# Kernel optimization log

Measured on AMD Instinct MI355X. Metric: run time of the kernel, lower is better.

## Reference

```python
import jax, jax.numpy as jnp
import numpy as np

EPISODES = 1_000_000


def setup_inputs() -> dict:
    key = jax.random.key(0)
    x = jax.random.normal(key, (1, EPISODES, 2), dtype=jnp.float32)
    return {"x": x}


def _rx_2x2(t):
    # expm(-i * t * X) = cos(t) I - i sin(t) X  (closed form for Pauli-X rotation)
    c = jnp.cos(t).astype(jnp.complex64)
    s = (-1j * jnp.sin(t).astype(jnp.complex64))
    row0 = jnp.stack([c, s], axis=-1)
    row1 = jnp.stack([s, c], axis=-1)
    return jnp.stack([row0, row1], axis=-2)  # (..., 2, 2)


def reference(x):
    # x: (1, E, 2) float32 -> angles a (qubit 1, X(x)I) and b (qubit 2, I(x)X)
    cnot = jnp.array([[1, 0, 0, 0],
                      [0, 1, 0, 0],
                      [0, 0, 0, 1],
                      [0, 0, 1, 0]], dtype=jnp.complex64)
    a = x[..., 0]  # (1, E)
    b = x[..., 1]  # (1, E)
    # sx1 = X(x)I and sx2 = I(x)X commute, so
    # expm(-i (a*sx1 + b*sx2)) = Rx(a) (x) Rx(b)  -- exact, replaces generic expm.
    Ra = _rx_2x2(a)  # (1, E, 2, 2)
    Rb = _rx_2x2(b)  # (1, E, 2, 2)
    # Kronecker product -> (1, E, 4, 4) complex64
    Rx = (Ra[..., :, None, :, None] * Rb[..., None, :, None, :]).reshape(
        a.shape[0], a.shape[1], 4, 4)
    propagator = jnp.einsum('iq,beqp->beip', cnot, Rx)  # (1, E, 4, 4)
    state_out = propagator[..., 0]                      # column 0 -> (1, E, 4)
    probabilities = jnp.square(jnp.abs(state_out)).astype(jnp.float32)
    logits = jnp.log(probabilities)                     # tf.log(prob) for multinomial
    # Vectorized categorical sampling over all episodes (replaces per-episode loop)
    skey = jax.random.key(42)
    choice = jax.random.categorical(skey, logits, axis=-1)  # (1, E) int
    # original: one_hot((1,1)) stacked on axis=1 -> (1, E, 1, 4)
    measurement = jax.nn.one_hot(choice, 4, dtype=jnp.float32)[:, :, None, :]
    return measurement
```

## Files before the change

### kernel.cpp

```cpp
#include <hip/hip_runtime.h>
#include <stdint.h>
#include <math.h>


#define N_EP 1000000

typedef float v2f __attribute__((ext_vector_type(2)));
#define V2(c) ((v2f){(c), (c)})

__device__ __forceinline__ uint32_t rotl32(uint32_t x, int d) {
  return (x << d) | (x >> (32 - d));
}

__device__ __forceinline__ void threefry(uint32_t x0, uint32_t x1,
                                         uint32_t& o0, uint32_t& o1) {
  const uint32_t k0 = 0u;
  const uint32_t k1 = 42u;
  const uint32_t k2 = (0u ^ 42u ^ 0x1BD11BDAu);
  x0 += k0; x1 += k1;
#define R4A { x0 += x1; x1 = rotl32(x1,13); x1 ^= x0; \
              x0 += x1; x1 = rotl32(x1,15); x1 ^= x0; \
              x0 += x1; x1 = rotl32(x1,26); x1 ^= x0; \
              x0 += x1; x1 = rotl32(x1, 6); x1 ^= x0; }
#define R4B { x0 += x1; x1 = rotl32(x1,17); x1 ^= x0; \
              x0 += x1; x1 = rotl32(x1,29); x1 ^= x0; \
              x0 += x1; x1 = rotl32(x1,16); x1 ^= x0; \
              x0 += x1; x1 = rotl32(x1,24); x1 ^= x0; }
  R4A; x0 += k1; x1 += k2 + 1u;
  R4B; x0 += k2; x1 += k0 + 2u;
  R4A; x0 += k0; x1 += k1 + 3u;
  R4B; x0 += k1; x1 += k2 + 4u;
  R4A; x0 += k2; x1 += k0 + 5u;
#undef R4A
#undef R4B
  o0 = x0; o1 = x1;
}


__device__ __forceinline__ v2f logf_xla2(v2f input) {
#pragma clang fp contract(off)
  const float kMinNorm = __uint_as_float(0x00800000u);
  uint32_t ubx = __float_as_uint(fmaxf(input.x, kMinNorm));
  uint32_t uby = __float_as_uint(fmaxf(input.y, kMinNorm));
  v2f e;
  e.x = (float)((int)(ubx >> 23) - 126);
  e.y = (float)((int)(uby >> 23) - 126);
  v2f x;
  x.x = __uint_as_float((ubx & 0x807fffffu) | 0x3f000000u);
  x.y = __uint_as_float((uby & 0x807fffffu) | 0x3f000000u);
  const float kSqrtHf = 0.707106781186547524f;
  bool mx = x.x < kSqrtHf;
  bool my = x.y < kSqrtHf;
  v2f tmp;
  tmp.x = mx ? x.x : 0.0f;
  tmp.y = my ? x.y : 0.0f;
  e.x = e.x - (mx ? 1.0f : 0.0f);
  e.y = e.y - (my ? 1.0f : 0.0f);
  x = x - V2(1.0f);
  x = x + tmp;
  v2f z = x * x;
  v2f y = V2(7.0376836292E-2f);
  y = y * x + V2(-1.1514610310E-1f);
  y = y * x + V2( 1.1676998740E-1f);
  y = y * x + V2(-1.2420140846E-1f);
  y = y * x + V2( 1.4249322787E-1f);
  y = y * x + V2(-1.6668057665E-1f);
  y = y * x + V2( 2.0000714765E-1f);
  y = y * x + V2(-2.4999993993E-1f);
  y = y * x + V2( 3.3333331174E-1f);
  y = y * x;
  y = y * z;
  y = e * V2(-2.12194440e-4f) + y;
  y = z * V2(-0.5f) + y;
  x = x + y;
  x = e * V2(0.693359375f) + x;
  if (input.x == 0.0f) x.x = -__builtin_inff();
  if (input.y == 0.0f) x.y = -__builtin_inff();
  return x;
}

__device__ __forceinline__ void sincosf_cr(float xf, float* sp, float* cp) {
  double x = (double)xf;
  double dn = __builtin_rint(x * 6.36619772367581382433e-01);
  int q = (int)dn;
  const double pio2_1  = 1.57079632673412561417e+00;
  const double pio2_1t = 6.07710050650619224932e-11;
  double r = fma(-dn, pio2_1, x);
  r = fma(-dn, pio2_1t, r);
  double z = r * r;
  double w = z * z;
  const double S1 = -1.66666666666666324348e-01;
  const double S2 =  8.33333333332248946124e-03;
  const double S3 = -1.98412698298579493134e-04;
  const double S4 =  2.75573137070700676789e-06;
  const double S5 = -2.50507602534068634195e-08;
  const double S6 =  1.58969099521155010221e-10;
  double rs = S2 + z * (S3 + z * S4) + z * w * (S5 + z * S6);
  double sinr = r + r * (z * (S1 + z * rs));
  const double C1 =  4.16666666666666019037e-02;
  const double C2 = -1.38888888888741095749e-03;
  const double C3 =  2.48015872894767294178e-05;
  const double C4 = -2.75573143513906633035e-07;
  const double C5 =  2.08757232129817482790e-09;
  const double C6 = -1.13596475577881948265e-11;
  double rc = z * (C1 + z * (C2 + z * C3)) + w * w * (C4 + z * (C5 + z * C6));
  double hz = 0.5 * z;
  double ww = 1.0 - hz;
  double cosr = ww + (((1.0 - ww) - hz) + z * rc);
  bool swap = q & 1;
  double s0 = swap ? cosr : sinr;
  double c0 = swap ? sinr : cosr;
  if (q & 2) s0 = -s0;
  if ((q + 1) & 2) c0 = -c0;
  *sp = (float)s0;
  *cp = (float)c0;
}

__device__ __forceinline__ float u_from_bits(uint32_t b) {
#pragma clang fp contract(off)
  const float tiny = 1.17549435e-38f;
  float f = __uint_as_float((b >> 9) | 0x3F800000u) - 1.0f;
  return fmaxf(tiny, f + tiny);
}

__device__ __forceinline__ v2f u2_from_bits(uint32_t b0, uint32_t b1) {
#pragma clang fp contract(off)
  const float tiny = 1.17549435e-38f;
  v2f f;
  f.x = __uint_as_float((b0 >> 9) | 0x3F800000u);
  f.y = __uint_as_float((b1 >> 9) | 0x3F800000u);
  f = f - V2(1.0f);
  f = f + V2(tiny);
  v2f u;
  u.x = fmaxf(tiny, f.x);
  u.y = fmaxf(tiny, f.y);
  return u;
}

__device__ __forceinline__ v2f gumbel2(uint32_t b0, uint32_t b1) {
  v2f u = u2_from_bits(b0, b1);
  v2f inner = logf_xla2(u);
  v2f outer = logf_xla2(-inner);
  return -outer;
}


__device__ __forceinline__ void fast_gumbel(uint32_t b, float* g, float* rtg) {
  const float LN2 = 0.6931471805599453f;
  float u = u_from_bits(b);
  float tg = -(LN2 * __builtin_amdgcn_logf(u));
  *g = -(LN2 * __builtin_amdgcn_logf(tg));
  *rtg = __builtin_amdgcn_rcpf(tg);
}

__global__ __launch_bounds__(256) void qcat_kernel(const float* __restrict__ x,
                                                   float* __restrict__ out) {
  int t = blockIdx.x * blockDim.x + threadIdx.x;
  if (t >= N_EP) return;

  uint32_t bits[4];
  uint32_t base = 4u * (uint32_t)t;
#pragma unroll
  for (int c = 0; c < 4; ++c) {
    uint32_t o0, o1;
    threefry(0u, base + (uint32_t)c, o0, o1);
    bits[c] = o0 ^ o1;
  }

  float2 ab = ((const float2*)x)[t];

  const float INV2PI = 0.15915494309189535f;
  const float LN2 = 0.6931471805599453f;
  float fra = __builtin_amdgcn_fractf(ab.x * INV2PI);
  float frb = __builtin_amdgcn_fractf(ab.y * INV2PI);
  float saf = __builtin_amdgcn_sinf(fra);
  float caf = __builtin_amdgcn_cosf(fra);
  float sbf = __builtin_amdgcn_sinf(frb);
  float cbf = __builtin_amdgcn_cosf(frb);
  float a0 = caf * cbf, a1 = caf * sbf, a2 = saf * sbf, a3 = saf * cbf;
  float p0 = a0 * a0, p1 = a1 * a1, p2 = a2 * a2, p3 = a3 * a3;
  float lp0 = LN2 * __builtin_amdgcn_logf(p0);
  float lp1 = LN2 * __builtin_amdgcn_logf(p1);
  float lp2 = LN2 * __builtin_amdgcn_logf(p2);
  float lp3 = LN2 * __builtin_amdgcn_logf(p3);
  float g0, g1, g2, g3, rtg0, rtg1, rtg2, rtg3;
  fast_gumbel(bits[0], &g0, &rtg0);
  fast_gumbel(bits[1], &g1, &rtg1);
  fast_gumbel(bits[2], &g2, &rtg2);
  fast_gumbel(bits[3], &g3, &rtg3);
  float y0 = lp0 + g0, y1 = lp1 + g1, y2 = lp2 + g2, y3 = lp3 + g3;

  const float K = 1.52587890625e-5f;
  float rta0 = __builtin_amdgcn_rcpf(fabsf(a0));
  float rta1 = __builtin_amdgcn_rcpf(fabsf(a1));
  float rta2 = __builtin_amdgcn_rcpf(fabsf(a2));
  float rta3 = __builtin_amdgcn_rcpf(fabsf(a3));
  float E0 = K * (fabsf(lp0) + fabsf(g0) + rtg0 + rta0 + 4.0f);
  float E1 = K * (fabsf(lp1) + fabsf(g1) + rtg1 + rta1 + 4.0f);
  float E2 = K * (fabsf(lp2) + fabsf(g2) + rtg2 + rta2 + 4.0f);
  float E3 = K * (fabsf(lp3) + fabsf(g3) + rtg3 + rta3 + 4.0f);
  float Emax = fmaxf(fmaxf(E0, E1), fmaxf(E2, E3));

  int   i01 = (y1 > y0) ? 1 : 0;
  float m01 = i01 ? y1 : y0;
  float s01 = i01 ? y0 : y1;
  int   i23 = (y3 > y2) ? 3 : 2;
  float m23 = i23 == 3 ? y3 : y2;
  float s23 = i23 == 3 ? y2 : y3;
  bool  sw  = m23 > m01;
  int   top = sw ? i23 : i01;
  float tv  = sw ? m23 : m01;
  float sv  = fmaxf(sw ? m01 : m23, sw ? s23 : s01);
  float margin = tv - sv;

  float pmin = fminf(fminf(p0, p1), fminf(p2, p3));
  bool safe = (margin > 2.0f * Emax) && (pmin >= 1.17549435e-38f);

  int best = top;
  if (!safe) {
#pragma clang fp contract(off)
    float ca, sa, cb, sb;
    sincosf_cr(ab.x, &sa, &ca);
    sincosf_cr(ab.y, &sb, &cb);
    v2f m0 = {ca, ca}, n0 = {cb, sb};
    v2f m1 = {sa, sa}, n1 = {sb, cb};
    v2f t01 = m0 * n0;
    v2f t23 = m1 * n1;
    v2f q01 = t01 * t01;
    v2f q23 = t23 * t23;
    v2f y01 = logf_xla2(q01) + gumbel2(bits[0], bits[1]);
    v2f y23 = logf_xla2(q23) + gumbel2(bits[2], bits[3]);
    int be = 0; float bv = y01.x;
    if (y01.y > bv) { bv = y01.y; be = 1; }
    if (y23.x > bv) { bv = y23.x; be = 2; }
    if (y23.y > bv) { bv = y23.y; be = 3; }
    best = be;
  }

  float4 o;
  o.x = (best == 0) ? 1.0f : 0.0f;
  o.y = (best == 1) ? 1.0f : 0.0f;
  o.z = (best == 2) ? 1.0f : 0.0f;
  o.w = (best == 3) ? 1.0f : 0.0f;
  ((float4*)out)[t] = o;
}

extern "C" void kernel_launch(void* const* d_in, const int* in_sizes, int n_in,
                              void* d_out, int out_size, void* d_ws, size_t ws_size,
                              hipStream_t stream) {
  const float* x = (const float*)d_in[0];
  float* out = (float*)d_out;
  dim3 block(256);
  dim3 grid((N_EP + 255) / 256);
  hipLaunchKernelGGL(qcat_kernel, grid, block, 0, stream, x, out);
}
```

Baseline: 73.28 us.

## Split unsafe episodes into atomic worklist and separate exact fixup kernel

The fast kernel no longer runs the exact double-precision sincos/log fallback inline. Instead it appends the indices of uncertain episodes to a workspace list through an atomic counter, and a separate fixup kernel recomputes only those episodes. The safety test also changes from a single global margin to per-pair error bounds, which should let more episodes count as safe. The aim is to remove divergent slow-path code and its register pressure from the main kernel. In exchange it adds two extra kernel launches and atomic contention, and the fixup grid of 64 blocks is fixed in size.

```diff
diff --git a/kernel.cpp b/kernel.cpp
--- a/kernel.cpp
+++ b/kernel.cpp
@@ -34,6 +34,13 @@
 #undef R4A
 #undef R4B
   o0 = x0; o1 = x1;
+}
+
+__device__ __forceinline__ float u_from_bits(uint32_t b) {
+#pragma clang fp contract(off)
+  const float tiny = 1.17549435e-38f;
+  float f = __uint_as_float((b >> 9) | 0x3F800000u) - 1.0f;
+  return fmaxf(tiny, f + tiny);
 }
 
 
@@ -116,13 +123,6 @@
   *cp = (float)c0;
 }
 
-__device__ __forceinline__ float u_from_bits(uint32_t b) {
-#pragma clang fp contract(off)
-  const float tiny = 1.17549435e-38f;
-  float f = __uint_as_float((b >> 9) | 0x3F800000u) - 1.0f;
-  return fmaxf(tiny, f + tiny);
-}
-
 __device__ __forceinline__ v2f u2_from_bits(uint32_t b0, uint32_t b1) {
 #pragma clang fp contract(off)
   const float tiny = 1.17549435e-38f;
@@ -145,16 +145,13 @@
 }
 
 
-__device__ __forceinline__ void fast_gumbel(uint32_t b, float* g, float* rtg) {
-  const float LN2 = 0.6931471805599453f;
-  float u = u_from_bits(b);
-  float tg = -(LN2 * __builtin_amdgcn_logf(u));
-  *g = -(LN2 * __builtin_amdgcn_logf(tg));
-  *rtg = __builtin_amdgcn_rcpf(tg);
-}
-
-__global__ __launch_bounds__(256) void qcat_kernel(const float* __restrict__ x,
-                                                   float* __restrict__ out) {
+__global__ void zero_ws(uint32_t* ws) {
+  if (blockIdx.x == 0 && threadIdx.x == 0) ws[0] = 0u;
+}
+
+__global__ __launch_bounds__(256) void fast_kernel(const float* __restrict__ x,
+                                                   float* __restrict__ out,
+                                                   uint32_t* __restrict__ ws) {
   int t = blockIdx.x * blockDim.x + threadIdx.x;
   if (t >= N_EP) return;
 
@@ -183,66 +180,99 @@
   float lp1 = LN2 * __builtin_amdgcn_logf(p1);
   float lp2 = LN2 * __builtin_amdgcn_logf(p2);
   float lp3 = LN2 * __builtin_amdgcn_logf(p3);
-  float g0, g1, g2, g3, rtg0, rtg1, rtg2, rtg3;
-  fast_gumbel(bits[0], &g0, &rtg0);
-  fast_gumbel(bits[1], &g1, &rtg1);
-  fast_gumbel(bits[2], &g2, &rtg2);
-  fast_gumbel(bits[3], &g3, &rtg3);
+
+  float u0 = u_from_bits(bits[0]);
+  float u1 = u_from_bits(bits[1]);
+  float u2 = u_from_bits(bits[2]);
+  float u3 = u_from_bits(bits[3]);
+  float tg0 = -(LN2 * __builtin_amdgcn_logf(u0));
+  float tg1 = -(LN2 * __builtin_amdgcn_logf(u1));
+  float tg2 = -(LN2 * __builtin_amdgcn_logf(u2));
+  float tg3 = -(LN2 * __builtin_amdgcn_logf(u3));
+  float g0 = -(LN2 * __builtin_amdgcn_logf(tg0));
+  float g1 = -(LN2 * __builtin_amdgcn_logf(tg1));
+  float g2 = -(LN2 * __builtin_amdgcn_logf(tg2));
+  float g3 = -(LN2 * __builtin_amdgcn_logf(tg3));
   float y0 = lp0 + g0, y1 = lp1 + g1, y2 = lp2 + g2, y3 = lp3 + g3;
 
   const float K = 1.52587890625e-5f;
-  float rta0 = __builtin_amdgcn_rcpf(fabsf(a0));
-  float rta1 = __builtin_amdgcn_rcpf(fabsf(a1));
-  float rta2 = __builtin_amdgcn_rcpf(fabsf(a2));
-  float rta3 = __builtin_amdgcn_rcpf(fabsf(a3));
-  float E0 = K * (fabsf(lp0) + fabsf(g0) + rtg0 + rta0 + 4.0f);
-  float E1 = K * (fabsf(lp1) + fabsf(g1) + rtg1 + rta1 + 4.0f);
-  float E2 = K * (fabsf(lp2) + fabsf(g2) + rtg2 + rta2 + 4.0f);
-  float E3 = K * (fabsf(lp3) + fabsf(g3) + rtg3 + rta3 + 4.0f);
-  float Emax = fmaxf(fmaxf(E0, E1), fmaxf(E2, E3));
-
-  int   i01 = (y1 > y0) ? 1 : 0;
-  float m01 = i01 ? y1 : y0;
-  float s01 = i01 ? y0 : y1;
-  int   i23 = (y3 > y2) ? 3 : 2;
-  float m23 = i23 == 3 ? y3 : y2;
-  float s23 = i23 == 3 ? y2 : y3;
-  bool  sw  = m23 > m01;
-  int   top = sw ? i23 : i01;
-  float tv  = sw ? m23 : m01;
-  float sv  = fmaxf(sw ? m01 : m23, sw ? s23 : s01);
-  float margin = tv - sv;
-
+  float E0 = K * (fabsf(lp0) + fabsf(g0) + __builtin_amdgcn_rcpf(tg0) +
+                  __builtin_amdgcn_rcpf(fabsf(a0)) + 4.0f);
+  float E1 = K * (fabsf(lp1) + fabsf(g1) + __builtin_amdgcn_rcpf(tg1) +
+                  __builtin_amdgcn_rcpf(fabsf(a1)) + 4.0f);
+  float E2 = K * (fabsf(lp2) + fabsf(g2) + __builtin_amdgcn_rcpf(tg2) +
+                  __builtin_amdgcn_rcpf(fabsf(a2)) + 4.0f);
+  float E3 = K * (fabsf(lp3) + fabsf(g3) + __builtin_amdgcn_rcpf(tg3) +
+                  __builtin_amdgcn_rcpf(fabsf(a3)) + 4.0f);
+
+  int best = 0; float bv = y0;
+  if (y1 > bv) { bv = y1; best = 1; }
+  if (y2 > bv) { bv = y2; best = 2; }
+  if (y3 > bv) { bv = y3; best = 3; }
+  float Eb = (best == 0) ? E0 : (best == 1) ? E1 : (best == 2) ? E2 : E3;
+
+  bool safe = true;
+  if (best != 0) safe = safe && (bv - y0 > Eb + E0);
+  if (best != 1) safe = safe && (bv - y1 > Eb + E1);
+  if (best != 2) safe = safe && (bv - y2 > Eb + E2);
+  if (best != 3) safe = safe && (bv - y3 > Eb + E3);
   float pmin = fminf(fminf(p0, p1), fminf(p2, p3));
-  bool safe = (margin > 2.0f * Emax) && (pmin >= 1.17549435e-38f);
-
-  int best = top;
-  if (!safe) {
-#pragma clang fp contract(off)
-    float ca, sa, cb, sb;
-    sincosf_cr(ab.x, &sa, &ca);
-    sincosf_cr(ab.y, &sb, &cb);
-    v2f m0 = {ca, ca}, n0 = {cb, sb};
-    v2f m1 = {sa, sa}, n1 = {sb, cb};
-    v2f t01 = m0 * n0;
-    v2f t23 = m1 * n1;
-    v2f q01 = t01 * t01;
-    v2f q23 = t23 * t23;
-    v2f y01 = logf_xla2(q01) + gumbel2(bits[0], bits[1]);
-    v2f y23 = logf_xla2(q23) + gumbel2(bits[2], bits[3]);
-    int be = 0; float bv = y01.x;
-    if (y01.y > bv) { bv = y01.y; be = 1; }
-    if (y23.x > bv) { bv = y23.x; be = 2; }
-    if (y23.y > bv) { bv = y23.y; be = 3; }
-    best = be;
+  safe = safe && (pmin >= 1.17549435e-38f);
+
+  if (safe) {
+    float4 o;
+    o.x = (best == 0) ? 1.0f : 0.0f;
+    o.y = (best == 1) ? 1.0f : 0.0f;
+    o.z = (best == 2) ? 1.0f : 0.0f;
+    o.w = (best == 3) ? 1.0f : 0.0f;
+    ((float4*)out)[t] = o;
+  } else {
+    uint32_t idx = atomicAdd(ws, 1u);
+    ws[4 + idx] = (uint32_t)t;
   }
-
-  float4 o;
-  o.x = (best == 0) ? 1.0f : 0.0f;
-  o.y = (best == 1) ? 1.0f : 0.0f;
-  o.z = (best == 2) ? 1.0f : 0.0f;
-  o.w = (best == 3) ? 1.0f : 0.0f;
-  ((float4*)out)[t] = o;
+}
+
+__global__ __launch_bounds__(256) void fixup_kernel(const float* __restrict__ x,
+                                                    float* __restrict__ out,
+                                                    const uint32_t* __restrict__ ws) {
+  uint32_t count = ws[0];
+  uint32_t stride = gridDim.x * blockDim.x;
+  for (uint32_t i = blockIdx.x * blockDim.x + threadIdx.x; i < count; i += stride) {
+    uint32_t t = ws[4 + i];
+    uint32_t bits[4];
+    uint32_t base = 4u * t;
+#pragma unroll
+    for (int c = 0; c < 4; ++c) {
+      uint32_t o0, o1;
+      threefry(0u, base + (uint32_t)c, o0, o1);
+      bits[c] = o0 ^ o1;
+    }
+    float2 ab = ((const float2*)x)[t];
+    {
+#pragma clang fp contract(off)
+      float ca, sa, cb, sb;
+      sincosf_cr(ab.x, &sa, &ca);
+      sincosf_cr(ab.y, &sb, &cb);
+      v2f m0 = {ca, ca}, n0 = {cb, sb};
+      v2f m1 = {sa, sa}, n1 = {sb, cb};
+      v2f t01 = m0 * n0;
+      v2f t23 = m1 * n1;
+      v2f q01 = t01 * t01;
+      v2f q23 = t23 * t23;
+      v2f y01 = logf_xla2(q01) + gumbel2(bits[0], bits[1]);
+      v2f y23 = logf_xla2(q23) + gumbel2(bits[2], bits[3]);
+      int be = 0; float bv = y01.x;
+      if (y01.y > bv) { bv = y01.y; be = 1; }
+      if (y23.x > bv) { bv = y23.x; be = 2; }
+      if (y23.y > bv) { bv = y23.y; be = 3; }
+      float4 o;
+      o.x = (be == 0) ? 1.0f : 0.0f;
+      o.y = (be == 1) ? 1.0f : 0.0f;
+      o.z = (be == 2) ? 1.0f : 0.0f;
+      o.w = (be == 3) ? 1.0f : 0.0f;
+      ((float4*)out)[t] = o;
+    }
+  }
 }
 
 extern "C" void kernel_launch(void* const* d_in, const int* in_sizes, int n_in,
@@ -250,7 +280,9 @@
                               hipStream_t stream) {
   const float* x = (const float*)d_in[0];
   float* out = (float*)d_out;
-  dim3 block(256);
-  dim3 grid((N_EP + 255) / 256);
-  hipLaunchKernelGGL(qcat_kernel, grid, block, 0, stream, x, out);
-}
+  uint32_t* ws = (uint32_t*)d_ws;
+  hipLaunchKernelGGL(zero_ws, dim3(1), dim3(64), 0, stream, ws);
+  hipLaunchKernelGGL(fast_kernel, dim3((N_EP + 255) / 256), dim3(256), 0, stream,
+                     x, out, ws);
+  hipLaunchKernelGGL(fixup_kernel, dim3(64), dim3(256), 0, stream, x, out, ws);
+}
```

Result: no change. 73.06 us (-0.3%).
